# Kernel optimization log

Hardware: AMD Instinct MI355X
Metric: run time of the kernel (lower is better)

The kernel has to match this reference:

```python
import jax, jax.numpy as jnp
import numpy as np

N_USERS = 100000
N_ITEMS = 50000
N_NODES = N_USERS + N_ITEMS
D = 64          # embedding_size / d_model
L = 2           # n_layers (GCN layers and transformer layers)
H = 8           # nhead
FF = 2048       # TransformerEncoderLayer default dim_feedforward
E_RAND = 1600000
B = 4096
EPS = 1e-5


def setup_inputs() -> dict:
    key = jax.random.key(0)
    ks = jax.random.split(key, 24)
    s = 0.05
    users = jax.random.randint(ks[0], (B,), 0, N_USERS)
    items = jax.random.randint(ks[1], (B,), 0, N_ITEMS)
    src = jax.random.randint(ks[2], (E_RAND,), 0, N_NODES)
    dst = jax.random.randint(ks[3], (E_RAND,), 0, N_NODES)
    loops = jnp.arange(N_NODES)  # ensure degree >= 1 everywhere (real graphs have no isolated rows)
    edge_index = jnp.stack([jnp.concatenate([src, loops]), jnp.concatenate([dst, loops])])
    f32 = jnp.float32
    return {
        "users": users,
        "items": items,
        "edge_index": edge_index,
        "user_table": jax.random.normal(ks[4], (N_USERS, D), f32) * s,
        "item_table": jax.random.normal(ks[5], (N_ITEMS, D), f32) * s,
        "gl_W": jax.random.normal(ks[6], (L, D, D), f32) * s,
        "gl_b": jax.random.normal(ks[7], (L, D), f32) * s,
        "corr_W": jax.random.normal(ks[8], (D, D), f32) * s,
        "corr_b": jax.random.normal(ks[9], (D,), f32) * s,
        "qkv_W": jax.random.normal(ks[10], (L, D, 3 * D), f32) * s,
        "qkv_b": jax.random.normal(ks[11], (L, 3 * D), f32) * s,
        "out_W": jax.random.normal(ks[12], (L, D, D), f32) * s,
        "out_b": jax.random.normal(ks[13], (L, D), f32) * s,
        "ff1_W": jax.random.normal(ks[14], (L, D, FF), f32) * s,
        "ff1_b": jax.random.normal(ks[15], (L, FF), f32) * s,
        "ff2_W": jax.random.normal(ks[16], (L, FF, D), f32) * s,
        "ff2_b": jax.random.normal(ks[17], (L, D), f32) * s,
        "ln1_g": jnp.ones((L, D), f32),
        "ln1_b": jnp.zeros((L, D), f32),
        "ln2_g": jnp.ones((L, D), f32),
        "ln2_b": jnp.zeros((L, D), f32),
    }


def _layer_norm(x, g, b):
    m = jnp.mean(x, axis=-1, keepdims=True)
    v = jnp.mean(jnp.square(x - m), axis=-1, keepdims=True)
    return (x - m) * jax.lax.rsqrt(v + EPS) * g + b


def _transformer(x, qkv_W, qkv_b, out_W, out_b, ff1_W, ff1_b, ff2_W, ff2_b,
                 ln1_g, ln1_b, ln2_g, ln2_b):
    # x: [N, D]; original passes x.unsqueeze(0) with batch_first=False -> seq_len=1,
    # batch=N. Softmax over a single key is identity, so MHA(x) == out_proj(V(x)).
    for l in range(L):
        v = x @ qkv_W[l][:, 2 * D:] + qkv_b[l][2 * D:]          # [N, D] value projection
        attn = v @ out_W[l] + out_b[l]
        x = _layer_norm(x + attn, ln1_g[l], ln1_b[l])            # post-LN (PyTorch default)
        ffn = jax.nn.relu(x @ ff1_W[l] + ff1_b[l]) @ ff2_W[l] + ff2_b[l]
        x = _layer_norm(x + ffn, ln2_g[l], ln2_b[l])
    return x


def reference(users, items, edge_index, user_table, item_table, gl_W, gl_b,
              corr_W, corr_b, qkv_W, qkv_b, out_W, out_b, ff1_W, ff1_b,
              ff2_W, ff2_b, ln1_g, ln1_b, ln2_g, ln2_b):
    row, col = edge_index[0], edge_index[1]
    # degree-normalized scatter-add GCN propagation (GraphLayer.message)
    deg = jax.ops.segment_sum(jnp.ones(row.shape, user_table.dtype), row, num_segments=N_NODES)
    dis = deg ** -0.5
    norm = dis[row] * dis[col]                                   # [E]
    x = jnp.concatenate([user_table, item_table], axis=0)        # [N_NODES, D]
    for l in range(L):
        h = x @ gl_W[l] + gl_b[l]
        msg = norm[:, None] * h[row]                             # gather + edge norm
        x = jax.ops.segment_sum(msg, col, num_segments=N_NODES)  # scatter-add aggr
    user_g, item_g = x[:N_USERS], x[N_USERS:]
    # CrossModalCorrection: one shared Linear on both
    user_c = user_g @ corr_W + corr_b
    item_c = item_g @ corr_W + corr_b
    tf = lambda z: _transformer(z, qkv_W, qkv_b, out_W, out_b, ff1_W, ff1_b,
                                ff2_W, ff2_b, ln1_g, ln1_b, ln2_g, ln2_b)
    user_final = tf(user_c)
    item_final = tf(item_c)
    return jnp.sum(user_final[users] * item_final[items], axis=1)  # [B]
```

## Files before the change

### kernel.cpp

```cpp
#include <hip/hip_runtime.h>
#include <math.h>

#define NU 100000
#define NI 50000
#define NN 150000
#define NNP 150528
#define SCNB 147
#define LNEPS 1e-5f

typedef short bfx8 __attribute__((ext_vector_type(8)));
typedef float f32x4 __attribute__((ext_vector_type(4)));
#define MFMA16(a, b, c) __builtin_amdgcn_mfma_f32_16x16x32_bf16(a, b, c, 0, 0, 0)

__device__ __forceinline__ unsigned short f2bf(float f) {
    unsigned u = __float_as_uint(f);
    unsigned r = u + 0x7FFFu + ((u >> 16) & 1u);
    return (unsigned short)(r >> 16);
}

__global__ __launch_bounds__(256) void k_markS(const int* __restrict__ users,
                                               const int* __restrict__ items,
                                               unsigned* __restrict__ bS, int nb) {
    int t = blockIdx.x * 256 + threadIdx.x;
    if (t < 2 * nb) {
        int node = (t < nb) ? users[t] : (NU + items[t - nb]);
        atomicOr(&bS[node >> 5], 1u << (node & 31));
    }
}

__global__ __launch_bounds__(256) void k_pre0(const int* __restrict__ row,
                                              const int* __restrict__ col,
                                              const unsigned* __restrict__ bS,
                                              int* __restrict__ deg,
                                              int* __restrict__ cnt,
                                              unsigned* __restrict__ bR, int E) {
    int e = blockIdx.x * 256 + threadIdx.x;
    if (e >= E) return;
    int r = row[e];
    int c = col[e];
    atomicAdd(&deg[r], 1);
    atomicAdd(&cnt[c], 1);
    if ((bS[c >> 5] >> (c & 31)) & 1u) atomicOr(&bR[r >> 5], 1u << (r & 31));
}

__global__ __launch_bounds__(256) void k_dis(const int* __restrict__ deg,
                                             float* __restrict__ dis) {
    int i = blockIdx.x * 256 + threadIdx.x;
    if (i < NN) dis[i] = rsqrtf((float)deg[i]);
}

__global__ __launch_bounds__(256) void k_scan1(const int* __restrict__ cnt,
                                               int* __restrict__ bsum) {
    __shared__ int sh[256];
    int b = blockIdx.x, t = threadIdx.x;
    int4 v = ((const int4*)cnt)[b * 256 + t];
    sh[t] = v.x + v.y + v.z + v.w;
    __syncthreads();
    for (int off = 128; off >= 1; off >>= 1) {
        if (t < off) sh[t] += sh[t + off];
        __syncthreads();
    }
    if (t == 0) bsum[b] = sh[0];
}

__global__ __launch_bounds__(256) void k_scan2(int* __restrict__ bsum, int nblk) {
    __shared__ int sh[256];
    int t = threadIdx.x;
    int v = (t < nblk) ? bsum[t] : 0;
    sh[t] = v;
    __syncthreads();
    for (int off = 1; off < 256; off <<= 1) {
        int add = (t >= off) ? sh[t - off] : 0;
        __syncthreads();
        sh[t] += add;
        __syncthreads();
    }
    if (t < nblk) bsum[t] = sh[t] - v;
}

__global__ __launch_bounds__(256) void k_scan3(const int* __restrict__ cnt,
                                               const int* __restrict__ bsum,
                                               int* __restrict__ start) {
    __shared__ int sh[257];
    int b = blockIdx.x, t = threadIdx.x;
    int4 v = ((const int4*)cnt)[b * 256 + t];
    int s = v.x + v.y + v.z + v.w;
    sh[t + 1] = s;
    if (t == 0) sh[0] = 0;
    __syncthreads();
    for (int off = 1; off < 256; off <<= 1) {
        int add = sh[t + 1] + ((t + 1 > off) ? sh[t + 1 - off] : 0);
        __syncthreads();
        sh[t + 1] = add;
        __syncthreads();
    }
    int base = bsum[b] + sh[t];
    int i0 = b * 1024 + t * 4;
    start[i0 + 0] = base;  base += v.x;
    start[i0 + 1] = base;  base += v.y;
    start[i0 + 2] = base;  base += v.z;
    start[i0 + 3] = base;
    if (b == SCNB - 1 && t == 255) start[NNP] = base + v.w;
}

__global__ __launch_bounds__(256) void k_place(const int* __restrict__ row,
                                               const int* __restrict__ col,
                                               const int* __restrict__ start,
                                               int* __restrict__ cur,
                                               int* __restrict__ el, int E) {
    int e = blockIdx.x * 256 + threadIdx.x;
    if (e >= E) return;
    int c = col[e];
    int pos = atomicAdd(&cur[c], 1);
    el[start[c] + pos] = row[e];
}

__global__ __launch_bounds__(256) void k_gather1(const int* __restrict__ el,
                                                 const int* __restrict__ start,
                                                 const float* __restrict__ dis,
                                                 const unsigned* __restrict__ filt,
                                                 const float* __restrict__ ut,
                                                 const float* __restrict__ itb,
                                                 float* __restrict__ g1,
                                                 float* __restrict__ sdeg) {
    int wid = (blockIdx.x * 256 + threadIdx.x) >> 6;
    int j = threadIdx.x & 63;
    if (wid >= NN) return;
    if (!((filt[wid >> 5] >> (wid & 31)) & 1u)) return;
    int s = start[wid], e = start[wid + 1];
    float a0 = 0.f, a1 = 0.f, a2 = 0.f, a3 = 0.f, sn = 0.f;
    int i = s;
    for (; i + 3 < e; i += 4) {
        int r0 = el[i], r1 = el[i + 1], r2 = el[i + 2], r3 = el[i + 3];
        float d0 = dis[r0], d1 = dis[r1], d2 = dis[r2], d3 = dis[r3];
        const float* p0 = (r0 < NU) ? ut + (size_t)r0 * 64 : itb + (size_t)(r0 - NU) * 64;
        const float* p1 = (r1 < NU) ? ut + (size_t)r1 * 64 : itb + (size_t)(r1 - NU) * 64;
        const float* p2 = (r2 < NU) ? ut + (size_t)r2 * 64 : itb + (size_t)(r2 - NU) * 64;
        const float* p3 = (r3 < NU) ? ut + (size_t)r3 * 64 : itb + (size_t)(r3 - NU) * 64;
        a0 = fmaf(d0, p0[j], a0);
        a1 = fmaf(d1, p1[j], a1);
        a2 = fmaf(d2, p2[j], a2);
        a3 = fmaf(d3, p3[j], a3);
        sn += (d0 + d1) + (d2 + d3);
    }
    for (; i < e; ++i) {
        int r0 = el[i];
        float d0 = dis[r0];
        const float* p0 = (r0 < NU) ? ut + (size_t)r0 * 64 : itb + (size_t)(r0 - NU) * 64;
        a0 = fmaf(d0, p0[j], a0);
        sn += d0;
    }
    float dc = dis[wid];
    g1[(size_t)wid * 64 + j] = dc * ((a0 + a1) + (a2 + a3));
    if (j == 0) sdeg[wid] = dc * sn;
}

__global__ __launch_bounds__(256) void k_gather2(const int* __restrict__ el,
                                                 const int* __restrict__ start,
                                                 const float* __restrict__ dis,
                                                 const unsigned* __restrict__ bS,
                                                 const float* __restrict__ g1,
                                                 const float* __restrict__ sdeg,
                                                 float* __restrict__ gg,
                                                 float* __restrict__ s2) {
    int wid = (blockIdx.x * 256 + threadIdx.x) >> 6;
    int j = threadIdx.x & 63;
    if (wid >= NN) return;
    if (!((bS[wid >> 5] >> (wid & 31)) & 1u)) return;
    int s = start[wid], e = start[wid + 1];
    float a0 = 0.f, a1 = 0.f, a2 = 0.f, a3 = 0.f, sa = 0.f;
    int i = s;
    for (; i + 3 < e; i += 4) {
        int r0 = el[i], r1 = el[i + 1], r2 = el[i + 2], r3 = el[i + 3];
        float d0 = dis[r0], d1 = dis[r1], d2 = dis[r2], d3 = dis[r3];
        a0 = fmaf(d0, g1[(size_t)r0 * 64 + j], a0);
        a1 = fmaf(d1, g1[(size_t)r1 * 64 + j], a1);
        a2 = fmaf(d2, g1[(size_t)r2 * 64 + j], a2);
        a3 = fmaf(d3, g1[(size_t)r3 * 64 + j], a3);
        sa = fmaf(d0, sdeg[r0], sa);
        sa = fmaf(d1, sdeg[r1], sa);
        sa = fmaf(d2, sdeg[r2], sa);
        sa = fmaf(d3, sdeg[r3], sa);
    }
    for (; i < e; ++i) {
        int r0 = el[i];
        float d0 = dis[r0];
        a0 = fmaf(d0, g1[(size_t)r0 * 64 + j], a0);
        sa = fmaf(d0, sdeg[r0], sa);
    }
    float dc = dis[wid];
    gg[(size_t)wid * 64 + j] = dc * ((a0 + a1) + (a2 + a3));
    if (j == 0) s2[wid] = dc * sa;
}

__global__ __launch_bounds__(256) void k_fuse(const float* __restrict__ qkvW,
                                              const float* __restrict__ qkvB,
                                              const float* __restrict__ outW,
                                              const float* __restrict__ outB,
                                              float* __restrict__ Wva,
                                              float* __restrict__ bva) {
    int l = blockIdx.x;
    __shared__ float wo[4096];
    int tid = threadIdx.x, j = tid & 63, kq = tid >> 6;
    for (int i = tid; i < 4096; i += 256) wo[i] = outW[l * 4096 + i];
    __syncthreads();
    for (int kk = 0; kk < 16; ++kk) {
        int k = kq * 16 + kk;
        float acc = 0.f;
        for (int m = 0; m < 64; ++m)
            acc = fmaf(qkvW[(size_t)l * 64 * 192 + k * 192 + 128 + m],
                       wo[m * 64 + j], acc);
        Wva[l * 4096 + k * 64 + j] = acc;
    }
    if (tid < 64) {
        float acc = outB[l * 64 + j];
        for (int m = 0; m < 64; ++m)
            acc = fmaf(qkvB[l * 192 + 128 + m], wo[m * 64 + j], acc);
        bva[l * 64 + j] = acc;
    }
}

__global__ __launch_bounds__(256) void k_fuse2(const float* __restrict__ glW,
                                               const float* __restrict__ glB,
                                               const float* __restrict__ corrW,
                                               const float* __restrict__ corrB,
                                               float* __restrict__ Wff,
                                               float* __restrict__ bff) {
    __shared__ float A[4096];
    __shared__ float B[4096];
    __shared__ float T[4096];
    __shared__ float vec[64];
    int tid = threadIdx.x, j = tid & 63, kq = tid >> 6;
    for (int i = tid; i < 4096; i += 256) { A[i] = glW[4096 + i]; B[i] = corrW[i]; }
    __syncthreads();
    for (int kk = 0; kk < 16; ++kk) {
        int k = kq * 16 + kk;
        float acc = 0.f;
        for (int m = 0; m < 64; ++m) acc = fmaf(glW[k * 64 + m], A[m * 64 + j], acc);
        T[k * 64 + j] = acc;
    }
    if (tid < 64) {
        float v = 0.f;
        for (int m = 0; m < 64; ++m) v = fmaf(glB[m], A[m * 64 + tid], v);
        vec[tid] = v;
    }
    __syncthreads();
    for (int kk = 0; kk < 16; ++kk) {
        int k = kq * 16 + kk;
        float acc = 0.f;
        for (int m = 0; m < 64; ++m) acc = fmaf(T[k * 64 + m], B[m * 64 + j], acc);
        Wff[k * 64 + j] = acc;
    }
    if (kq == 0) {
        float a = 0.f;
        for (int m = 0; m < 64; ++m) a = fmaf(vec[m], B[m * 64 + j], a);
        bff[j] = a;
    } else if (kq == 1) {
        float a = 0.f;
        for (int m = 0; m < 64; ++m) a = fmaf(glB[64 + m], B[m * 64 + j], a);
        bff[64 + j] = a;
    } else if (kq == 2) {
        bff[128 + j] = corrB[j];
    }
}

__global__ __launch_bounds__(256) void k_wprep(const float* __restrict__ ff1W,
                                               const float* __restrict__ ff2W,
                                               unsigned short* __restrict__ Wt1,
                                               unsigned short* __restrict__ Wt2) {
    __shared__ float sh[64][65];
    int b = blockIdx.x;
    int l = b >> 6, rem = b & 63;
    int mat = rem >> 5, tile = rem & 31;
    const float* src; unsigned short* dst; int C, R, r0, c0;
    if (mat == 0) { src = ff1W + (size_t)l * 64 * 2048; dst = Wt1 + (size_t)l * 2048 * 64;
                    R = 64; C = 2048; r0 = 0; c0 = tile * 64; }
    else          { src = ff2W + (size_t)l * 2048 * 64; dst = Wt2 + (size_t)l * 64 * 2048;
                    R = 2048; C = 64; r0 = tile * 64; c0 = 0; }
    int tid = threadIdx.x;
    for (int it = 0; it < 16; ++it) {
        int idx = it * 256 + tid;
        int lr = idx >> 6, lc = idx & 63;
        sh[lr][lc] = src[(size_t)(r0 + lr) * C + (c0 + lc)];
    }
    __syncthreads();
    for (int it = 0; it < 16; ++it) {
        int idx = it * 256 + tid;
        int lc = idx >> 6, lr = idx & 63;
        dst[(size_t)(c0 + lc) * R + (r0 + lr)] = f2bf(sh[lr][lc]);
    }
}

__global__ __launch_bounds__(256) void k_proj(const float* __restrict__ gg,
                                              const float* __restrict__ sdeg,
                                              const float* __restrict__ s2,
                                              const int* __restrict__ users,
                                              const int* __restrict__ items,
                                              const float* __restrict__ Wff,
                                              const float* __restrict__ bff,
                                              float* __restrict__ Cb, int nb) {
    __shared__ float Ws[4096];
    __shared__ float xsh[16][64];
    __shared__ float ssh[16][2];
    int tid = threadIdx.x, j = tid & 63, rq = tid >> 6;
    for (int i = tid; i < 4096; i += 256) Ws[i] = Wff[i];
    int r0 = blockIdx.x * 16;
    for (int i = tid; i < 1024; i += 256) {
        int b = r0 + (i >> 6);
        int node = (b < nb) ? users[b] : (NU + items[b - nb]);
        xsh[i >> 6][i & 63] = gg[(size_t)node * 64 + (i & 63)];
    }
    if (tid < 16) {
        int b = r0 + tid;
        int node = (b < nb) ? users[b] : (NU + items[b - nb]);
        ssh[tid][0] = s2[node];
        ssh[tid][1] = sdeg[node];
    }
    __syncthreads();
    float b1j = bff[j], b2j = bff[64 + j], cbj = bff[128 + j];
    float acc[4];
#pragma unroll
    for (int i = 0; i < 4; ++i) acc[i] = cbj;
    for (int k = 0; k < 64; ++k) {
        float w = Ws[k * 64 + j];
#pragma unroll
        for (int i = 0; i < 4; ++i) acc[i] = fmaf(xsh[rq + 4 * i][k], w, acc[i]);
    }
#pragma unroll
    for (int i = 0; i < 4; ++i) {
        int r = rq + 4 * i;
        Cb[(size_t)(r0 + r) * 64 + j] = acc[i] + ssh[r][0] * b1j + ssh[r][1] * b2j;
    }
}

__global__ __launch_bounds__(256) void k_attn(float* __restrict__ Cb,
                                              unsigned short* __restrict__ xb,
                                              const float* __restrict__ Wva,
                                              const float* __restrict__ bva,
                                              const float* __restrict__ g,
                                              const float* __restrict__ bt,
                                              int layer) {
    __shared__ float Ws[4096];
    __shared__ float xs[16][64];
    int tid = threadIdx.x, j = tid & 63, rq = tid >> 6;
    const float* wv = Wva + layer * 4096;
    for (int i = tid; i < 4096; i += 256) Ws[i] = wv[i];
    int row0 = blockIdx.x * 16;
    for (int i = tid; i < 1024; i += 256)
        xs[i >> 6][i & 63] = Cb[(size_t)(row0 + (i >> 6)) * 64 + (i & 63)];
    __syncthreads();
    float bv = bva[layer * 64 + j];
    float gg = g[layer * 64 + j], bb = bt[layer * 64 + j];
    float acc[4];
#pragma unroll
    for (int i = 0; i < 4; ++i) acc[i] = bv;
    for (int k = 0; k < 64; ++k) {
        float w = Ws[k * 64 + j];
#pragma unroll
        for (int i = 0; i < 4; ++i) acc[i] = fmaf(xs[rq * 4 + i][k], w, acc[i]);
    }
#pragma unroll
    for (int i = 0; i < 4; ++i) {
        int r = rq * 4 + i;
        float xv = xs[r][j] + acc[i];
        float s = xv;
#pragma unroll
        for (int o = 32; o >= 1; o >>= 1) s += __shfl_xor(s, o, 64);
        float m = s * (1.0f / 64.0f);
        float d = xv - m;
        float s2v = d * d;
#pragma unroll
        for (int o = 32; o >= 1; o >>= 1) s2v += __shfl_xor(s2v, o, 64);
        float xn = d * rsqrtf(s2v * (1.0f / 64.0f) + LNEPS) * gg + bb;
        Cb[(size_t)(row0 + r) * 64 + j] = xn;
        xb[(size_t)(row0 + r) * 64 + j] = f2bf(xn);
    }
}

__global__ __launch_bounds__(512) void k_ffnm(float* __restrict__ Cb,
                                              const unsigned short* __restrict__ xb,
                                              const unsigned short* __restrict__ Wt1,
                                              const unsigned short* __restrict__ Wt2,
                                              const float* __restrict__ ff1B,
                                              const float* __restrict__ ff2B,
                                              const float* __restrict__ g2,
                                              const float* __restrict__ b2t,
                                              int layer) {
    __shared__ short ts[2][32 * 128];
    __shared__ float ys[32 * 64];
    const unsigned short* w1 = Wt1 + (size_t)layer * 2048 * 64;
    const unsigned short* w2 = Wt2 + (size_t)layer * 64 * 2048;
    const float* b1 = ff1B + layer * 2048;
    int tid = threadIdx.x;
    int lane = tid & 63, wv = tid >> 6;
    int g = lane >> 4, r16 = lane & 15;
    int row0 = blockIdx.x * 32;
    int nt2 = wv & 3, mh = wv >> 2;

    bfx8 ax[2][2];
#pragma unroll
    for (int mt = 0; mt < 2; ++mt)
#pragma unroll
        for (int ks = 0; ks < 2; ++ks)
            ax[mt][ks] = *(const bfx8*)(xb + ((size_t)(row0 + 16 * mt + r16)) * 64
                                        + 32 * ks + 8 * g);

    f32x4 yfA = {0.f, 0.f, 0.f, 0.f}, yfB = {0.f, 0.f, 0.f, 0.f};
    int col = wv * 16 + r16;
    int trow = 16 * mh + r16;

    for (int hc2 = 0; hc2 < 8; ++hc2) {
        bfx8 w2f[2][4];
#pragma unroll
        for (int sub = 0; sub < 2; ++sub)
#pragma unroll
            for (int ks2 = 0; ks2 < 4; ++ks2)
                w2f[sub][ks2] = *(const bfx8*)(w2 + ((size_t)(16 * nt2 + r16)) * 2048
                                               + (hc2 * 2 + sub) * 128
                                               + 32 * ks2 + 8 * g);
#pragma unroll
        for (int sub = 0; sub < 2; ++sub) {
            int h = (hc2 * 2 + sub) * 128 + wv * 16 + r16;
            float b1v = b1[h];
            f32x4 tf0 = {b1v, b1v, b1v, b1v}, tf1 = tf0;
#pragma unroll
            for (int ks = 0; ks < 2; ++ks) {
                bfx8 bw = *(const bfx8*)(w1 + (size_t)h * 64 + 32 * ks + 8 * g);
                tf0 = MFMA16(ax[0][ks], bw, tf0);
                tf1 = MFMA16(ax[1][ks], bw, tf1);
            }
#pragma unroll
            for (int r = 0; r < 4; ++r) {
                int rowA = 4 * g + r, rowB = 16 + 4 * g + r;
                int offA = (rowA * 256 + col * 2) ^ ((rowA & 7) << 4);
                int offB = (rowB * 256 + col * 2) ^ ((rowB & 7) << 4);
                *(short*)((char*)ts[sub] + offA) = (short)f2bf(fmaxf(tf0[r], 0.f));
                *(short*)((char*)ts[sub] + offB) = (short)f2bf(fmaxf(tf1[r], 0.f));
            }
        }
        __syncthreads();
#pragma unroll
        for (int sub = 0; sub < 2; ++sub)
#pragma unroll
            for (int ks2 = 0; ks2 < 4; ++ks2) {
                int kl = 32 * ks2 + 8 * g;
                int off2 = (trow * 256 + kl * 2) ^ ((trow & 7) << 4);
                bfx8 ta = *(const bfx8*)((char*)ts[sub] + off2);
                if (ks2 & 1) yfB = MFMA16(ta, w2f[sub][ks2], yfB);
                else         yfA = MFMA16(ta, w2f[sub][ks2], yfA);
            }
        __syncthreads();
    }
#pragma unroll
    for (int r = 0; r < 4; ++r)
        ys[(16 * mh + 4 * g + r) * 64 + 16 * nt2 + r16] = yfA[r] + yfB[r];
    __syncthreads();
    float b2 = ff2B[layer * 64 + lane];
    float gg = g2[layer * 64 + lane], bb = b2t[layer * 64 + lane];
#pragma unroll
    for (int i = 0; i < 4; ++i) {
        int r = wv * 4 + i;
        float xv = Cb[(size_t)(row0 + r) * 64 + lane] + ys[r * 64 + lane] + b2;
        float s = xv;
#pragma unroll
        for (int o = 32; o >= 1; o >>= 1) s += __shfl_xor(s, o, 64);
        float m = s * (1.0f / 64.0f);
        float d = xv - m;
        float s2v = d * d;
#pragma unroll
        for (int o = 32; o >= 1; o >>= 1) s2v += __shfl_xor(s2v, o, 64);
        float xn = d * rsqrtf(s2v * (1.0f / 64.0f) + LNEPS) * gg + bb;
        Cb[(size_t)(row0 + r) * 64 + lane] = xn;
    }
}

__global__ __launch_bounds__(256) void k_dot(const float* __restrict__ Cb,
                                             float* __restrict__ out, int nb) {
    int t = blockIdx.x * 256 + threadIdx.x;
    int b = t >> 4;
    if (b >= nb) return;
    int q = (t & 15) * 4;
    const float4 u = *reinterpret_cast<const float4*>(Cb + (size_t)b * 64 + q);
    const float4 v = *reinterpret_cast<const float4*>(Cb + (size_t)(nb + b) * 64 + q);
    float s = u.x * v.x + u.y * v.y + u.z * v.z + u.w * v.w;
#pragma unroll
    for (int o = 8; o >= 1; o >>= 1) s += __shfl_xor(s, o, 16);
    if ((t & 15) == 0) out[b] = s;
}

extern "C" void kernel_launch(void* const* d_in, const int* in_sizes, int n_in,
                              void* d_out, int out_size, void* d_ws, size_t ws_size,
                              hipStream_t stream) {
    const int* users = (const int*)d_in[0];
    const int* items = (const int*)d_in[1];
    const int* ei    = (const int*)d_in[2];
    const float* ut  = (const float*)d_in[3];
    const float* itb = (const float*)d_in[4];
    const float* glW = (const float*)d_in[5];
    const float* glB = (const float*)d_in[6];
    const float* corrW = (const float*)d_in[7];
    const float* corrB = (const float*)d_in[8];
    const float* qkvW = (const float*)d_in[9];
    const float* qkvB = (const float*)d_in[10];
    const float* outW = (const float*)d_in[11];
    const float* outB = (const float*)d_in[12];
    const float* ff1W = (const float*)d_in[13];
    const float* ff1B = (const float*)d_in[14];
    const float* ff2W = (const float*)d_in[15];
    const float* ff2B = (const float*)d_in[16];
    const float* ln1g = (const float*)d_in[17];
    const float* ln1b = (const float*)d_in[18];
    const float* ln2g = (const float*)d_in[19];
    const float* ln2b = (const float*)d_in[20];

    const int E  = in_sizes[2] / 2;
    const int nb = in_sizes[0];
    const int nrows = 2 * nb;
    const int* rowp = ei;
    const int* colp = ei + E;

    char* w = (char*)d_ws;
    size_t off = 0;
    auto alloc = [&](size_t bytes) {
        char* p = w + off;
        off += (bytes + 255) & ~(size_t)255;
        return p;
    };
    int*      deg   = (int*)alloc((size_t)NN * 4);
    float*    dis   = (float*)alloc((size_t)NN * 4);
    unsigned* bS    = (unsigned*)alloc(((NN + 31) / 32) * 4);
    unsigned* bR    = (unsigned*)alloc(((NN + 31) / 32) * 4);
    int*      cnt   = (int*)alloc((size_t)NNP * 4);
    int*      start = (int*)alloc((size_t)(NNP + 1) * 4);
    int*      cur   = (int*)alloc((size_t)NN * 4);
    int*      bsum  = (int*)alloc((size_t)SCNB * 4);
    int*      el    = (int*)alloc((size_t)E * 4);
    float*    bufA  = (float*)alloc((size_t)NN * 64 * 4);
    float*    bufB  = (float*)alloc((size_t)NN * 64 * 4);
    float*    sdeg  = (float*)alloc((size_t)NN * 4);
    float*    s2    = (float*)alloc((size_t)NN * 4);
    float*    cb    = (float*)alloc((size_t)nrows * 64 * 4);
    float*    Wva   = (float*)alloc(2 * 4096 * 4);
    float*    bva   = (float*)alloc(2 * 64 * 4);
    float*    Wff   = (float*)alloc(4096 * 4);
    float*    bff   = (float*)alloc(192 * 4);
    unsigned short* xbb = (unsigned short*)alloc((size_t)nrows * 64 * 2);
    unsigned short* Wt1 = (unsigned short*)alloc((size_t)2 * 2048 * 64 * 2);
    unsigned short* Wt2 = (unsigned short*)alloc((size_t)2 * 64 * 2048 * 2);
    float*    outp  = (float*)d_out;

    hipMemsetAsync(deg, 0, (size_t)NN * 4, stream);
    hipMemsetAsync(bS, 0, ((NN + 31) / 32) * 4, stream);
    hipMemsetAsync(bR, 0, ((NN + 31) / 32) * 4, stream);
    hipMemsetAsync(cnt, 0, (size_t)NNP * 4, stream);
    hipMemsetAsync(cur, 0, (size_t)NN * 4, stream);

    int eb = (E + 255) / 256;
    int nnb = (NN + 255) / 256;

    k_markS<<<(2 * nb + 255) / 256, 256, 0, stream>>>(users, items, bS, nb);
    k_pre0<<<eb, 256, 0, stream>>>(rowp, colp, bS, deg, cnt, bR, E);
    k_dis<<<nnb, 256, 0, stream>>>(deg, dis);
    k_scan1<<<SCNB, 256, 0, stream>>>(cnt, bsum);
    k_scan2<<<1, 256, 0, stream>>>(bsum, SCNB);
    k_scan3<<<SCNB, 256, 0, stream>>>(cnt, bsum, start);
    k_place<<<eb, 256, 0, stream>>>(rowp, colp, start, cur, el, E);
    k_fuse<<<2, 256, 0, stream>>>(qkvW, qkvB, outW, outB, Wva, bva);
    k_fuse2<<<1, 256, 0, stream>>>(glW, glB, corrW, corrB, Wff, bff);
    k_wprep<<<128, 256, 0, stream>>>(ff1W, ff2W, Wt1, Wt2);

    int agb = (NN + 3) / 4;

    k_gather1<<<agb, 256, 0, stream>>>(el, start, dis, bR, ut, itb, bufA, sdeg);
    k_gather2<<<agb, 256, 0, stream>>>(el, start, dis, bS, bufA, sdeg, bufB, s2);
    k_proj<<<(nrows + 15) / 16, 256, 0, stream>>>(bufB, sdeg, s2, users, items,
                                                  Wff, bff, cb, nb);

    for (int l = 0; l < 2; ++l) {
        k_attn<<<nrows / 16, 256, 0, stream>>>(cb, xbb, Wva, bva, ln1g, ln1b, l);
        k_ffnm<<<nrows / 32, 512, 0, stream>>>(cb, xbb, Wt1, Wt2, ff1B, ff2B,
                                               ln2g, ln2b, l);
    }
    k_dot<<<(nb * 16 + 255) / 256, 256, 0, stream>>>(cb, outp, nb);
}
```

Baseline: 574.6 us.

## Partition edge atomics by node-range owner blocks and build CSR only for needed rows

```diff
diff --git a/kernel.cpp b/kernel.cpp
--- a/kernel.cpp
+++ b/kernel.cpp
@@ -7,6 +7,8 @@
 #define NNP 150528
 #define SCNB 147
 #define LNEPS 1e-5f
+#define NOWN 8
+#define OWNSZ 18752
 
 typedef short bfx8 __attribute__((ext_vector_type(8)));
 typedef float f32x4 __attribute__((ext_vector_type(4)));
@@ -28,19 +30,25 @@
     }
 }
 
-__global__ __launch_bounds__(256) void k_pre0(const int* __restrict__ row,
-                                              const int* __restrict__ col,
-                                              const unsigned* __restrict__ bS,
-                                              int* __restrict__ deg,
-                                              int* __restrict__ cnt,
-                                              unsigned* __restrict__ bR, int E) {
-    int e = blockIdx.x * 256 + threadIdx.x;
-    if (e >= E) return;
-    int r = row[e];
-    int c = col[e];
-    atomicAdd(&deg[r], 1);
-    atomicAdd(&cnt[c], 1);
-    if ((bS[c >> 5] >> (c & 31)) & 1u) atomicOr(&bR[r >> 5], 1u << (r & 31));
+__global__ __launch_bounds__(256) void k_edgeA(const int* __restrict__ row,
+                                               const int* __restrict__ col,
+                                               const unsigned* __restrict__ bS,
+                                               int* __restrict__ deg,
+                                               int* __restrict__ cnt,
+                                               unsigned* __restrict__ bR, int E) {
+    int grp = blockIdx.x & (NOWN - 1);
+    int lo = grp * OWNSZ;
+    int hi = lo + OWNSZ; if (hi > NN) hi = NN;
+    int stride = (gridDim.x >> 3) * 256;
+    for (int e = (blockIdx.x >> 3) * 256 + threadIdx.x; e < E; e += stride) {
+        int r = row[e];
+        int c = col[e];
+        bool rown = (r >= lo) && (r < hi);
+        if (rown) atomicAdd(&deg[r], 1);
+        if (c >= lo && c < hi) atomicAdd(&cnt[c], 1);
+        if (rown && ((bS[c >> 5] >> (c & 31)) & 1u))
+            atomicOr(&bR[r >> 5], 1u << (r & 31));
+    }
 }
 
 __global__ __launch_bounds__(256) void k_dis(const int* __restrict__ deg,
@@ -50,11 +58,18 @@
 }
 
 __global__ __launch_bounds__(256) void k_scan1(const int* __restrict__ cnt,
+                                               const unsigned* __restrict__ bR,
                                                int* __restrict__ bsum) {
     __shared__ int sh[256];
     int b = blockIdx.x, t = threadIdx.x;
+    int i0 = b * 1024 + t * 4;
     int4 v = ((const int4*)cnt)[b * 256 + t];
-    sh[t] = v.x + v.y + v.z + v.w;
+    unsigned wb = bR[i0 >> 5] >> (i0 & 31);
+    int m0 = (wb & 1u) ? v.x : 0;
+    int m1 = (wb & 2u) ? v.y : 0;
+    int m2 = (wb & 4u) ? v.z : 0;
+    int m3 = (wb & 8u) ? v.w : 0;
+    sh[t] = m0 + m1 + m2 + m3;
     __syncthreads();
     for (int off = 128; off >= 1; off >>= 1) {
         if (t < off) sh[t] += sh[t + off];
@@ -79,12 +94,19 @@
 }
 
 __global__ __launch_bounds__(256) void k_scan3(const int* __restrict__ cnt,
+                                               const unsigned* __restrict__ bR,
                                                const int* __restrict__ bsum,
                                                int* __restrict__ start) {
     __shared__ int sh[257];
     int b = blockIdx.x, t = threadIdx.x;
+    int i0 = b * 1024 + t * 4;
     int4 v = ((const int4*)cnt)[b * 256 + t];
-    int s = v.x + v.y + v.z + v.w;
+    unsigned wb = bR[i0 >> 5] >> (i0 & 31);
+    int m0 = (wb & 1u) ? v.x : 0;
+    int m1 = (wb & 2u) ? v.y : 0;
+    int m2 = (wb & 4u) ? v.z : 0;
+    int m3 = (wb & 8u) ? v.w : 0;
+    int s = m0 + m1 + m2 + m3;
     sh[t + 1] = s;
     if (t == 0) sh[0] = 0;
     __syncthreads();
@@ -95,24 +117,31 @@
         __syncthreads();
     }
     int base = bsum[b] + sh[t];
-    int i0 = b * 1024 + t * 4;
-    start[i0 + 0] = base;  base += v.x;
-    start[i0 + 1] = base;  base += v.y;
-    start[i0 + 2] = base;  base += v.z;
+    start[i0 + 0] = base;  base += m0;
+    start[i0 + 1] = base;  base += m1;
+    start[i0 + 2] = base;  base += m2;
     start[i0 + 3] = base;
-    if (b == SCNB - 1 && t == 255) start[NNP] = base + v.w;
-}
-
-__global__ __launch_bounds__(256) void k_place(const int* __restrict__ row,
-                                               const int* __restrict__ col,
-                                               const int* __restrict__ start,
-                                               int* __restrict__ cur,
-                                               int* __restrict__ el, int E) {
-    int e = blockIdx.x * 256 + threadIdx.x;
-    if (e >= E) return;
-    int c = col[e];
-    int pos = atomicAdd(&cur[c], 1);
-    el[start[c] + pos] = row[e];
+    if (b == SCNB - 1 && t == 255) start[NNP] = base + m3;
+}
+
+__global__ __launch_bounds__(256) void k_placeO(const int* __restrict__ row,
+                                                const int* __restrict__ col,
+                                                const unsigned* __restrict__ bR,
+                                                const int* __restrict__ start,
+                                                int* __restrict__ cur,
+                                                int* __restrict__ el, int E) {
+    int grp = blockIdx.x & (NOWN - 1);
+    int lo = grp * OWNSZ;
+    int hi = lo + OWNSZ; if (hi > NN) hi = NN;
+    int stride = (gridDim.x >> 3) * 256;
+    for (int e = (blockIdx.x >> 3) * 256 + threadIdx.x; e < E; e += stride) {
+        int c = col[e];
+        int r = row[e];
+        if (c < lo || c >= hi) continue;
+        if (!((bR[c >> 5] >> (c & 31)) & 1u)) continue;
+        int pos = atomicAdd(&cur[c], 1);
+        el[start[c] + pos] = r;
+    }
 }
 
 __global__ __launch_bounds__(256) void k_gather1(const int* __restrict__ el,
@@ -526,13 +555,15 @@
         off += (bytes + 255) & ~(size_t)255;
         return p;
     };
+    size_t zero0 = off;
     int*      deg   = (int*)alloc((size_t)NN * 4);
+    int*      cnt   = (int*)alloc((size_t)NNP * 4);
+    int*      cur   = (int*)alloc((size_t)NN * 4);
+    unsigned* bS    = (unsigned*)alloc((NNP / 32) * 4);
+    unsigned* bR    = (unsigned*)alloc((NNP / 32) * 4);
+    size_t zlen = off - zero0;
     float*    dis   = (float*)alloc((size_t)NN * 4);
-    unsigned* bS    = (unsigned*)alloc(((NN + 31) / 32) * 4);
-    unsigned* bR    = (unsigned*)alloc(((NN + 31) / 32) * 4);
-    int*      cnt   = (int*)alloc((size_t)NNP * 4);
     int*      start = (int*)alloc((size_t)(NNP + 1) * 4);
-    int*      cur   = (int*)alloc((size_t)NN * 4);
     int*      bsum  = (int*)alloc((size_t)SCNB * 4);
     int*      el    = (int*)alloc((size_t)E * 4);
     float*    bufA  = (float*)alloc((size_t)NN * 64 * 4);
@@ -549,22 +580,18 @@
     unsigned short* Wt2 = (unsigned short*)alloc((size_t)2 * 64 * 2048 * 2);
     float*    outp  = (float*)d_out;
 
-    hipMemsetAsync(deg, 0, (size_t)NN * 4, stream);
-    hipMemsetAsync(bS, 0, ((NN + 31) / 32) * 4, stream);
-    hipMemsetAsync(bR, 0, ((NN + 31) / 32) * 4, stream);
-    hipMemsetAsync(cnt, 0, (size_t)NNP * 4, stream);
-    hipMemsetAsync(cur, 0, (size_t)NN * 4, stream);
-
-    int eb = (E + 255) / 256;
+    hipMemsetAsync(w + zero0, 0, zlen, stream);
+
     int nnb = (NN + 255) / 256;
+    int egrid = 1024;
 
     k_markS<<<(2 * nb + 255) / 256, 256, 0, stream>>>(users, items, bS, nb);
-    k_pre0<<<eb, 256, 0, stream>>>(rowp, colp, bS, deg, cnt, bR, E);
+    k_edgeA<<<egrid, 256, 0, stream>>>(rowp, colp, bS, deg, cnt, bR, E);
     k_dis<<<nnb, 256, 0, stream>>>(deg, dis);
-    k_scan1<<<SCNB, 256, 0, stream>>>(cnt, bsum);
+    k_scan1<<<SCNB, 256, 0, stream>>>(cnt, bR, bsum);
     k_scan2<<<1, 256, 0, stream>>>(bsum, SCNB);
-    k_scan3<<<SCNB, 256, 0, stream>>>(cnt, bsum, start);
-    k_place<<<eb, 256, 0, stream>>>(rowp, colp, start, cur, el, E);
+    k_scan3<<<SCNB, 256, 0, stream>>>(cnt, bR, bsum, start);
+    k_placeO<<<egrid, 256, 0, stream>>>(rowp, colp, bR, start, cur, el, E);
     k_fuse<<<2, 256, 0, stream>>>(qkvW, qkvB, outW, outB, Wva, bva);
     k_fuse2<<<1, 256, 0, stream>>>(glW, glB, corrW, corrB, Wff, bff);
     k_wprep<<<128, 256, 0, stream>>>(ff1W, ff2W, Wt1, Wt2);
```

Result: faster. 519.3 us (-9.6%).

## Replace global-atomic degree/count histogram and CSR placement with LDS-privatized range histograms

Applied to the files above, without the earlier changes.

```diff
diff --git a/kernel.cpp b/kernel.cpp
--- a/kernel.cpp
+++ b/kernel.cpp
@@ -7,6 +7,9 @@
 #define NNP 150528
 #define SCNB 147
 #define LNEPS 1e-5f
+#define RSZ 8192
+#define NR 19
+#define BCH 16
 
 typedef short bfx8 __attribute__((ext_vector_type(8)));
 typedef float f32x4 __attribute__((ext_vector_type(4)));
@@ -28,25 +31,72 @@
     }
 }
 
-__global__ __launch_bounds__(256) void k_pre0(const int* __restrict__ row,
+__global__ __launch_bounds__(256) void k_hist(const int* __restrict__ row,
                                               const int* __restrict__ col,
                                               const unsigned* __restrict__ bS,
-                                              int* __restrict__ deg,
-                                              int* __restrict__ cnt,
-                                              unsigned* __restrict__ bR, int E) {
-    int e = blockIdx.x * 256 + threadIdx.x;
-    if (e >= E) return;
-    int r = row[e];
-    int c = col[e];
-    atomicAdd(&deg[r], 1);
-    atomicAdd(&cnt[c], 1);
-    if ((bS[c >> 5] >> (c & 31)) & 1u) atomicOr(&bR[r >> 5], 1u << (r & 31));
-}
-
-__global__ __launch_bounds__(256) void k_dis(const int* __restrict__ deg,
-                                             float* __restrict__ dis) {
+                                              int* __restrict__ pdeg,
+                                              int* __restrict__ pcnt,
+                                              unsigned* __restrict__ bR,
+                                              int E, int ech) {
+    __shared__ int h[RSZ];
+    __shared__ unsigned bb[RSZ / 32];
+    int b = blockIdx.x, r = blockIdx.y, mode = blockIdx.z;
+    int lo = r * RSZ;
+    int lim = NNP - lo; if (lim > RSZ) lim = RSZ;
+    int tid = threadIdx.x;
+    for (int i = tid; i < RSZ; i += 256) h[i] = 0;
+    if (mode == 0)
+        for (int i = tid; i < RSZ / 32; i += 256) bb[i] = 0;
+    __syncthreads();
+    int e0 = b * ech, e1 = e0 + ech; if (e1 > E) e1 = E;
+    if (mode == 0) {
+        for (int e = e0 + tid; e < e1; e += 256) {
+            int rr = row[e];
+            unsigned idx = (unsigned)(rr - lo);
+            if (idx < (unsigned)RSZ) {
+                atomicAdd(&h[idx], 1);
+                int c = col[e];
+                if ((bS[c >> 5] >> (c & 31)) & 1u)
+                    atomicOr(&bb[idx >> 5], 1u << (idx & 31));
+            }
+        }
+    } else {
+        for (int e = e0 + tid; e < e1; e += 256) {
+            int c = col[e];
+            unsigned idx = (unsigned)(c - lo);
+            if (idx < (unsigned)RSZ) atomicAdd(&h[idx], 1);
+        }
+    }
+    __syncthreads();
+    int* dst = (mode == 0 ? pdeg : pcnt) + (size_t)b * NNP + lo;
+    for (int i = tid; i < lim; i += 256) dst[i] = h[i];
+    if (mode == 0) {
+        int wlim = (lim + 31) >> 5;
+        for (int i = tid; i < wlim; i += 256) {
+            unsigned v = bb[i];
+            if (v) atomicOr(&bR[(lo >> 5) + i], v);
+        }
+    }
+}
+
+__global__ __launch_bounds__(256) void k_reduce(const int* __restrict__ pdeg,
+                                                int* __restrict__ pcnt,
+                                                float* __restrict__ dis,
+                                                int* __restrict__ cnt) {
     int i = blockIdx.x * 256 + threadIdx.x;
-    if (i < NN) dis[i] = rsqrtf((float)deg[i]);
+    if (i >= NNP) return;
+    int d = 0;
+#pragma unroll
+    for (int b = 0; b < BCH; ++b) d += pdeg[(size_t)b * NNP + i];
+    if (i < NN) dis[i] = rsqrtf((float)d);
+    int acc = 0;
+#pragma unroll
+    for (int b = 0; b < BCH; ++b) {
+        int v = pcnt[(size_t)b * NNP + i];
+        pcnt[(size_t)b * NNP + i] = acc;
+        acc += v;
+    }
+    cnt[i] = acc;
 }
 
 __global__ __launch_bounds__(256) void k_scan1(const int* __restrict__ cnt,
@@ -103,16 +153,29 @@
     if (b == SCNB - 1 && t == 255) start[NNP] = base + v.w;
 }
 
-__global__ __launch_bounds__(256) void k_place(const int* __restrict__ row,
-                                               const int* __restrict__ col,
-                                               const int* __restrict__ start,
-                                               int* __restrict__ cur,
-                                               int* __restrict__ el, int E) {
-    int e = blockIdx.x * 256 + threadIdx.x;
-    if (e >= E) return;
-    int c = col[e];
-    int pos = atomicAdd(&cur[c], 1);
-    el[start[c] + pos] = row[e];
+__global__ __launch_bounds__(256) void k_placeH(const int* __restrict__ row,
+                                                const int* __restrict__ col,
+                                                const int* __restrict__ start,
+                                                const int* __restrict__ pre,
+                                                int* __restrict__ el,
+                                                int E, int ech) {
+    __shared__ int cur[RSZ];
+    int b = blockIdx.x, r = blockIdx.y;
+    int lo = r * RSZ;
+    int lim = NNP - lo; if (lim > RSZ) lim = RSZ;
+    int tid = threadIdx.x;
+    const int* prb = pre + (size_t)b * NNP + lo;
+    for (int i = tid; i < lim; i += 256) cur[i] = start[lo + i] + prb[i];
+    __syncthreads();
+    int e0 = b * ech, e1 = e0 + ech; if (e1 > E) e1 = E;
+    for (int e = e0 + tid; e < e1; e += 256) {
+        int c = col[e];
+        unsigned idx = (unsigned)(c - lo);
+        if (idx < (unsigned)lim) {
+            int slot = atomicAdd(&cur[idx], 1);
+            el[slot] = row[e];
+        }
+    }
 }
 
 __global__ __launch_bounds__(256) void k_gather1(const int* __restrict__ el,
@@ -516,6 +579,7 @@
     const int E  = in_sizes[2] / 2;
     const int nb = in_sizes[0];
     const int nrows = 2 * nb;
+    const int ech = (E + BCH - 1) / BCH;
     const int* rowp = ei;
     const int* colp = ei + E;
 
@@ -526,13 +590,13 @@
         off += (bytes + 255) & ~(size_t)255;
         return p;
     };
-    int*      deg   = (int*)alloc((size_t)NN * 4);
+    size_t zero0 = off;
+    unsigned* bS    = (unsigned*)alloc((NNP / 32) * 4);
+    unsigned* bR    = (unsigned*)alloc((NNP / 32) * 4);
+    size_t zlen = off - zero0;
     float*    dis   = (float*)alloc((size_t)NN * 4);
-    unsigned* bS    = (unsigned*)alloc(((NN + 31) / 32) * 4);
-    unsigned* bR    = (unsigned*)alloc(((NN + 31) / 32) * 4);
     int*      cnt   = (int*)alloc((size_t)NNP * 4);
     int*      start = (int*)alloc((size_t)(NNP + 1) * 4);
-    int*      cur   = (int*)alloc((size_t)NN * 4);
     int*      bsum  = (int*)alloc((size_t)SCNB * 4);
     int*      el    = (int*)alloc((size_t)E * 4);
     float*    bufA  = (float*)alloc((size_t)NN * 64 * 4);
@@ -548,23 +612,20 @@
     unsigned short* Wt1 = (unsigned short*)alloc((size_t)2 * 2048 * 64 * 2);
     unsigned short* Wt2 = (unsigned short*)alloc((size_t)2 * 64 * 2048 * 2);
     float*    outp  = (float*)d_out;
-
-    hipMemsetAsync(deg, 0, (size_t)NN * 4, stream);
-    hipMemsetAsync(bS, 0, ((NN + 31) / 32) * 4, stream);
-    hipMemsetAsync(bR, 0, ((NN + 31) / 32) * 4, stream);
-    hipMemsetAsync(cnt, 0, (size_t)NNP * 4, stream);
-    hipMemsetAsync(cur, 0, (size_t)NN * 4, stream);
-
-    int eb = (E + 255) / 256;
-    int nnb = (NN + 255) / 256;
+    int* pdeg = (int*)bufA;
+    int* pcnt = pdeg + (size_t)BCH * NNP;
+
+    hipMemsetAsync(w + zero0, 0, zlen, stream);
 
     k_markS<<<(2 * nb + 255) / 256, 256, 0, stream>>>(users, items, bS, nb);
-    k_pre0<<<eb, 256, 0, stream>>>(rowp, colp, bS, deg, cnt, bR, E);
-    k_dis<<<nnb, 256, 0, stream>>>(deg, dis);
+    dim3 hgrid(BCH, NR, 2);
+    k_hist<<<hgrid, 256, 0, stream>>>(rowp, colp, bS, pdeg, pcnt, bR, E, ech);
+    k_reduce<<<NNP / 256, 256, 0, stream>>>(pdeg, pcnt, dis, cnt);
     k_scan1<<<SCNB, 256, 0, stream>>>(cnt, bsum);
     k_scan2<<<1, 256, 0, stream>>>(bsum, SCNB);
     k_scan3<<<SCNB, 256, 0, stream>>>(cnt, bsum, start);
-    k_place<<<eb, 256, 0, stream>>>(rowp, colp, start, cur, el, E);
+    dim3 pgrid(BCH, NR);
+    k_placeH<<<pgrid, 256, 0, stream>>>(rowp, colp, start, pcnt, el, E, ech);
     k_fuse<<<2, 256, 0, stream>>>(qkvW, qkvB, outW, outB, Wva, bva);
     k_fuse2<<<1, 256, 0, stream>>>(glW, glB, corrW, corrB, Wff, bff);
     k_wprep<<<128, 256, 0, stream>>>(ff1W, ff2W, Wt1, Wt2);
```

Result: slower. 814.1 us (+41.7%).

## Build CSR only for nodes needed by sampled rows; vectorize FFN hidden stores

Applied to the files above, without the earlier changes.

```diff
diff --git a/kernel.cpp b/kernel.cpp
--- a/kernel.cpp
+++ b/kernel.cpp
@@ -28,25 +28,35 @@
     }
 }
 
-__global__ __launch_bounds__(256) void k_pre0(const int* __restrict__ row,
+__global__ __launch_bounds__(256) void k_pre1(const int* __restrict__ row,
                                               const int* __restrict__ col,
                                               const unsigned* __restrict__ bS,
                                               int* __restrict__ deg,
-                                              int* __restrict__ cnt,
-                                              unsigned* __restrict__ bR, int E) {
+                                              unsigned* bR, int E) {
     int e = blockIdx.x * 256 + threadIdx.x;
     if (e >= E) return;
     int r = row[e];
+    atomicAdd(&deg[r], 1);
     int c = col[e];
-    atomicAdd(&deg[r], 1);
-    atomicAdd(&cnt[c], 1);
-    if ((bS[c >> 5] >> (c & 31)) & 1u) atomicOr(&bR[r >> 5], 1u << (r & 31));
+    if ((bS[c >> 5] >> (c & 31)) & 1u) {
+        unsigned m = 1u << (r & 31);
+        if (!(bR[r >> 5] & m)) atomicOr(&bR[r >> 5], m);
+    }
 }
 
 __global__ __launch_bounds__(256) void k_dis(const int* __restrict__ deg,
                                              float* __restrict__ dis) {
     int i = blockIdx.x * 256 + threadIdx.x;
     if (i < NN) dis[i] = rsqrtf((float)deg[i]);
+}
+
+__global__ __launch_bounds__(256) void k_cnt(const int* __restrict__ col,
+                                             const unsigned* __restrict__ bR,
+                                             int* __restrict__ cnt, int E) {
+    int e = blockIdx.x * 256 + threadIdx.x;
+    if (e >= E) return;
+    int c = col[e];
+    if ((bR[c >> 5] >> (c & 31)) & 1u) atomicAdd(&cnt[c], 1);
 }
 
 __global__ __launch_bounds__(256) void k_scan1(const int* __restrict__ cnt,
@@ -105,12 +115,14 @@
 
 __global__ __launch_bounds__(256) void k_place(const int* __restrict__ row,
                                                const int* __restrict__ col,
+                                               const unsigned* __restrict__ bR,
                                                const int* __restrict__ start,
                                                int* __restrict__ cur,
                                                int* __restrict__ el, int E) {
     int e = blockIdx.x * 256 + threadIdx.x;
     if (e >= E) return;
     int c = col[e];
+    if (!((bR[c >> 5] >> (c & 31)) & 1u)) return;
     int pos = atomicAdd(&cur[c], 1);
     el[start[c] + pos] = row[e];
 }
@@ -406,7 +418,6 @@
                                         + 32 * ks + 8 * g);
 
     f32x4 yfA = {0.f, 0.f, 0.f, 0.f}, yfB = {0.f, 0.f, 0.f, 0.f};
-    int col = wv * 16 + r16;
     int trow = 16 * mh + r16;
 
     for (int hc2 = 0; hc2 < 8; ++hc2) {
@@ -420,23 +431,31 @@
                                                + 32 * ks2 + 8 * g);
 #pragma unroll
         for (int sub = 0; sub < 2; ++sub) {
-            int h = (hc2 * 2 + sub) * 128 + wv * 16 + r16;
-            float b1v = b1[h];
-            f32x4 tf0 = {b1v, b1v, b1v, b1v}, tf1 = tf0;
+            int hbase = (hc2 * 2 + sub) * 128 + wv * 16;
+            f32x4 tf0 = *(const f32x4*)(b1 + hbase + 4 * g);
+            f32x4 tf1 = tf0;
 #pragma unroll
             for (int ks = 0; ks < 2; ++ks) {
-                bfx8 bw = *(const bfx8*)(w1 + (size_t)h * 64 + 32 * ks + 8 * g);
-                tf0 = MFMA16(ax[0][ks], bw, tf0);
-                tf1 = MFMA16(ax[1][ks], bw, tf1);
+                bfx8 bw = *(const bfx8*)(w1 + (size_t)(hbase + r16) * 64
+                                         + 32 * ks + 8 * g);
+                tf0 = MFMA16(bw, ax[0][ks], tf0);
+                tf1 = MFMA16(bw, ax[1][ks], tf1);
             }
-#pragma unroll
-            for (int r = 0; r < 4; ++r) {
-                int rowA = 4 * g + r, rowB = 16 + 4 * g + r;
-                int offA = (rowA * 256 + col * 2) ^ ((rowA & 7) << 4);
-                int offB = (rowB * 256 + col * 2) ^ ((rowB & 7) << 4);
-                *(short*)((char*)ts[sub] + offA) = (short)f2bf(fmaxf(tf0[r], 0.f));
-                *(short*)((char*)ts[sub] + offB) = (short)f2bf(fmaxf(tf1[r], 0.f));
-            }
+            int hb2 = (wv * 16 + 4 * g) * 2;
+            short4 sv0, sv1;
+            sv0.x = (short)f2bf(fmaxf(tf0[0], 0.f));
+            sv0.y = (short)f2bf(fmaxf(tf0[1], 0.f));
+            sv0.z = (short)f2bf(fmaxf(tf0[2], 0.f));
+            sv0.w = (short)f2bf(fmaxf(tf0[3], 0.f));
+            sv1.x = (short)f2bf(fmaxf(tf1[0], 0.f));
+            sv1.y = (short)f2bf(fmaxf(tf1[1], 0.f));
+            sv1.z = (short)f2bf(fmaxf(tf1[2], 0.f));
+            sv1.w = (short)f2bf(fmaxf(tf1[3], 0.f));
+            int rA = r16, rB = 16 + r16;
+            int offA = (rA * 256 + hb2) ^ ((rA & 7) << 4);
+            int offB = (rB * 256 + hb2) ^ ((rB & 7) << 4);
+            *(short4*)((char*)ts[sub] + offA) = sv0;
+            *(short4*)((char*)ts[sub] + offB) = sv1;
         }
         __syncthreads();
 #pragma unroll
@@ -526,13 +545,15 @@
         off += (bytes + 255) & ~(size_t)255;
         return p;
     };
+    size_t zero0 = off;
     int*      deg   = (int*)alloc((size_t)NN * 4);
+    int*      cnt   = (int*)alloc((size_t)NNP * 4);
+    int*      cur   = (int*)alloc((size_t)NN * 4);
+    unsigned* bS    = (unsigned*)alloc((NNP / 32) * 4);
+    unsigned* bR    = (unsigned*)alloc((NNP / 32) * 4);
+    size_t zlen = off - zero0;
     float*    dis   = (float*)alloc((size_t)NN * 4);
-    unsigned* bS    = (unsigned*)alloc(((NN + 31) / 32) * 4);
-    unsigned* bR    = (unsigned*)alloc(((NN + 31) / 32) * 4);
-    int*      cnt   = (int*)alloc((size_t)NNP * 4);
     int*      start = (int*)alloc((size_t)(NNP + 1) * 4);
-    int*      cur   = (int*)alloc((size_t)NN * 4);
     int*      bsum  = (int*)alloc((size_t)SCNB * 4);
     int*      el    = (int*)alloc((size_t)E * 4);
     float*    bufA  = (float*)alloc((size_t)NN * 64 * 4);
@@ -549,22 +570,19 @@
     unsigned short* Wt2 = (unsigned short*)alloc((size_t)2 * 64 * 2048 * 2);
     float*    outp  = (float*)d_out;
 
-    hipMemsetAsync(deg, 0, (size_t)NN * 4, stream);
-    hipMemsetAsync(bS, 0, ((NN + 31) / 32) * 4, stream);
-    hipMemsetAsync(bR, 0, ((NN + 31) / 32) * 4, stream);
-    hipMemsetAsync(cnt, 0, (size_t)NNP * 4, stream);
-    hipMemsetAsync(cur, 0, (size_t)NN * 4, stream);
+    hipMemsetAsync(w + zero0, 0, zlen, stream);
 
     int eb = (E + 255) / 256;
     int nnb = (NN + 255) / 256;
 
     k_markS<<<(2 * nb + 255) / 256, 256, 0, stream>>>(users, items, bS, nb);
-    k_pre0<<<eb, 256, 0, stream>>>(rowp, colp, bS, deg, cnt, bR, E);
+    k_pre1<<<eb, 256, 0, stream>>>(rowp, colp, bS, deg, bR, E);
     k_dis<<<nnb, 256, 0, stream>>>(deg, dis);
+    k_cnt<<<eb, 256, 0, stream>>>(colp, bR, cnt, E);
     k_scan1<<<SCNB, 256, 0, stream>>>(cnt, bsum);
     k_scan2<<<1, 256, 0, stream>>>(bsum, SCNB);
     k_scan3<<<SCNB, 256, 0, stream>>>(cnt, bsum, start);
-    k_place<<<eb, 256, 0, stream>>>(rowp, colp, start, cur, el, E);
+    k_place<<<eb, 256, 0, stream>>>(rowp, colp, bR, start, cur, el, E);
     k_fuse<<<2, 256, 0, stream>>>(qkvW, qkvB, outW, outB, Wva, bva);
     k_fuse2<<<1, 256, 0, stream>>>(glW, glB, corrW, corrB, Wff, bff);
     k_wprep<<<128, 256, 0, stream>>>(ff1W, ff2W, Wt1, Wt2);
```

Result: faster. 482.8 us (-16.0%).
